# Optimization experiments

Measured on AMD Instinct MI355X. Metric: run time of the kernel, lower is better.

## Reference

```python
import jax, jax.numpy as jnp
import numpy as np

D_IN = 1024
D_OUT = 1024

def setup_inputs() -> dict:
    key = jax.random.key(0)
    ks = jax.random.split(key, 7)
    s = 1.0 / np.sqrt(D_IN)
    x = jax.random.normal(ks[0], (4, 2048, D_IN), dtype=jnp.float32)
    Wq = jax.random.uniform(ks[1], (D_IN, D_OUT), jnp.float32, -s, s)
    Wk = jax.random.uniform(ks[2], (D_IN, D_OUT), jnp.float32, -s, s)
    Wv = jax.random.uniform(ks[3], (D_IN, D_OUT), jnp.float32, -s, s)
    bq = jax.random.uniform(ks[4], (D_OUT,), jnp.float32, -s, s)
    bk = jax.random.uniform(ks[5], (D_OUT,), jnp.float32, -s, s)
    bv = jax.random.uniform(ks[6], (D_OUT,), jnp.float32, -s, s)
    return {"x": x, "Wq": Wq, "Wk": Wk, "Wv": Wv, "bq": bq, "bk": bk, "bv": bv}

def reference(x, Wq, Wk, Wv, bq, bk, bv):
    # x: [b, n, d_in]
    q = jnp.einsum('bnd,de->bne', x, Wq) + bq
    k = jnp.einsum('bnd,de->bne', x, Wk) + bk
    v = jnp.einsum('bnd,de->bne', x, Wv) + bv
    scale = 1.0 / jnp.sqrt(jnp.asarray(k.shape[-1], dtype=x.dtype))
    scores = jnp.einsum('bqe,bke->bqk', q, k) * scale  # [b, n, n]
    weights = jax.nn.softmax(scores, axis=-1)
    return jnp.einsum('bqk,bke->bqe', weights, v)
```

## Files before the change

kernel.cpp:

```cpp
#include <hip/hip_runtime.h>
#include <cstdint>

typedef __bf16 bf16x8 __attribute__((ext_vector_type(8)));
typedef float f32x16 __attribute__((ext_vector_type(16)));

__device__ __forceinline__ unsigned short f2b(float f) {
    union { float f; uint32_t u; } x; x.f = f;
    uint32_t r = (x.u + 0x7fffu + ((x.u >> 16) & 1u)) >> 16;
    return (unsigned short)r;
}
__device__ __forceinline__ float b2f(unsigned short h) {
    union { float f; uint32_t u; } x; x.u = ((uint32_t)h) << 16;
    return x.f;
}

__global__ __launch_bounds__(256) void prep_kernel(const float* __restrict__ x,
                                                   unsigned short* __restrict__ xb,
                                                   const float* __restrict__ Wq,
                                                   const float* __restrict__ Wk,
                                                   const float* __restrict__ Wv,
                                                   unsigned short* __restrict__ Wt) {
    const int bid = blockIdx.x;
    const int tid = threadIdx.x;
    if (bid < 8192) {
        int i = (bid * 256 + tid) * 4;
        float4 v = *(const float4*)(x + i);
        ushort4 o;
        o.x = f2b(v.x); o.y = f2b(v.y); o.z = f2b(v.z); o.w = f2b(v.w);
        *(ushort4*)(xb + i) = o;
    } else {
        __shared__ float tile[32][33];
        const int b = bid - 8192;
        const int z = b >> 10;
        const int rem = b & 1023;
        const int n0 = (rem & 31) * 32;
        const int k0 = (rem >> 5) * 32;
        const float* W = (z == 0) ? Wq : (z == 1) ? Wk : Wv;
        const int tx = tid & 31, ty4 = tid >> 5;
#pragma unroll
        for (int i = 0; i < 4; ++i)
            tile[ty4 * 4 + i][tx] = W[(k0 + ty4 * 4 + i) * 1024 + n0 + tx];
        __syncthreads();
#pragma unroll
        for (int i = 0; i < 4; ++i) {
            const int row = ty4 * 4 + i;
            Wt[((long)z * 1024 + n0 + row) * 1024 + k0 + tx] = f2b(tile[tx][row]);
        }
    }
}

template <int EPI>
__global__ __launch_bounds__(256) void gemm32(const unsigned short* __restrict__ A, int lda, long sA,
                                              const unsigned short* __restrict__ Bm, int ldb, long sB,
                                              void* __restrict__ Cv, long sC, int K,
                                              const float* __restrict__ bq, const float* __restrict__ bk,
                                              const float* __restrict__ bv,
                                              unsigned short* __restrict__ Qb,
                                              unsigned short* __restrict__ Kb,
                                              unsigned short* __restrict__ Vt) {
    __shared__ unsigned short As0[128 * 64];
    __shared__ unsigned short Bs0[128 * 64];
    __shared__ unsigned short As1[128 * 64];
    __shared__ unsigned short Bs1[128 * 64];

    const int tid = threadIdx.x;
    const int wave = tid >> 6, lane = tid & 63;
    const int h = lane >> 5;
    const int l31 = lane & 31;
    const int wm = wave >> 1, wn = wave & 1;
    const long bm = (long)blockIdx.y * 128;
    const long bn = (long)blockIdx.x * 128;

    const unsigned short* Ab = A + (long)blockIdx.z * sA;
    const unsigned short* Bb = Bm + (long)blockIdx.z * sB;

    f32x16 acc[2][2];
#pragma unroll
    for (int mi = 0; mi < 2; ++mi) {
#pragma unroll
        for (int ni = 0; ni < 2; ++ni) {
#pragma unroll
            for (int r = 0; r < 16; ++r) acc[mi][ni][r] = 0.0f;
        }
    }

    const int srow_in = lane >> 3;
    const int cswz = (lane & 7) ^ srow_in;
    const unsigned short* aptr[4];
    const unsigned short* bptr[4];
    int sloff[4];
#pragma unroll
    for (int j = 0; j < 4; ++j) {
        const int row = j * 32 + wave * 8 + srow_in;
        aptr[j] = Ab + (bm + row) * (long)lda + cswz * 8;
        bptr[j] = Bb + (bn + row) * (long)ldb + cswz * 8;
        sloff[j] = (j * 32 + wave * 8) * 64;
    }

    const int arow0 = (wm * 64 + l31) * 64;
    const int brow0 = (wn * 64 + l31) * 64;
    int sw[4];
#pragma unroll
    for (int kh = 0; kh < 4; ++kh)
        sw[kh] = (((2 * kh + h) ^ (lane & 7)) * 8);

#define STAGE(AsB, BsB, kofs)                                                                           \
    do {                                                                                                \
        _Pragma("unroll")                                                                               \
        for (int j = 0; j < 4; ++j) {                                                                   \
            __builtin_amdgcn_global_load_lds(                                                           \
                (const __attribute__((address_space(1))) void*)(aptr[j] + (kofs)),                      \
                (__attribute__((address_space(3))) void*)(&AsB[sloff[j]]), 16, 0, 0);                   \
            __builtin_amdgcn_global_load_lds(                                                           \
                (const __attribute__((address_space(1))) void*)(bptr[j] + (kofs)),                      \
                (__attribute__((address_space(3))) void*)(&BsB[sloff[j]]), 16, 0, 0);                   \
        }                                                                                               \
    } while (0)

#define COMPUTE_T(AsB, BsB)                                                                             \
    do {                                                                                                \
        _Pragma("unroll")                                                                               \
        for (int kp = 0; kp < 2; ++kp) {                                                                \
            bf16x8 af[2][2], bfr[2][2];                                                                 \
            _Pragma("unroll")                                                                           \
            for (int mi = 0; mi < 2; ++mi) {                                                            \
                _Pragma("unroll")                                                                       \
                for (int kk = 0; kk < 2; ++kk) {                                                        \
                    af[mi][kk] = *(const bf16x8*)&AsB[arow0 + mi * 32 * 64 + sw[kp * 2 + kk]];          \
                }                                                                                       \
            }                                                                                           \
            _Pragma("unroll")                                                                           \
            for (int ni = 0; ni < 2; ++ni) {                                                            \
                _Pragma("unroll")                                                                       \
                for (int kk = 0; kk < 2; ++kk) {                                                        \
                    bfr[ni][kk] = *(const bf16x8*)&BsB[brow0 + ni * 32 * 64 + sw[kp * 2 + kk]];         \
                }                                                                                       \
            }                                                                                           \
            _Pragma("unroll")                                                                           \
            for (int kk = 0; kk < 2; ++kk) {                                                            \
                _Pragma("unroll")                                                                       \
                for (int mi = 0; mi < 2; ++mi) {                                                        \
                    _Pragma("unroll")                                                                   \
                    for (int ni = 0; ni < 2; ++ni) {                                                    \
                        acc[mi][ni] = __builtin_amdgcn_mfma_f32_32x32x16_bf16(af[mi][kk], bfr[ni][kk],  \
                                                                              acc[mi][ni], 0, 0, 0);    \
                    }                                                                                   \
                }                                                                                       \
            }                                                                                           \
        }                                                                                               \
    } while (0)

    STAGE(As0, Bs0, 0);

    for (int k0 = 0; k0 < K; k0 += 128) {
        __syncthreads();
        STAGE(As1, Bs1, k0 + 64);
        COMPUTE_T(As0, Bs0);
        __syncthreads();
        if (k0 + 128 < K) STAGE(As0, Bs0, k0 + 128);
        COMPUTE_T(As1, Bs1);
    }

#undef STAGE
#undef COMPUTE_T

#pragma unroll
    for (int mi = 0; mi < 2; ++mi) {
#pragma unroll
        for (int ni = 0; ni < 2; ++ni) {
            const f32x16 a = acc[mi][ni];
            const long col = bn + wn * 64 + ni * 32 + l31;
            const long rowB = bm + wm * 64 + mi * 32 + h * 4;
            if constexpr (EPI == 0) {
                if (col < 1024) {
                    const float bias = bq[col];
#pragma unroll
                    for (int g = 0; g < 4; ++g) {
#pragma unroll
                        for (int r = 0; r < 4; ++r)
                            Qb[(rowB + g * 8 + r) * 1024 + col] = f2b((a[g * 4 + r] + bias) * 0.03125f);
                    }
                } else if (col < 2048) {
                    const float bias = bk[col - 1024];
#pragma unroll
                    for (int g = 0; g < 4; ++g) {
#pragma unroll
                        for (int r = 0; r < 4; ++r)
                            Kb[(rowB + g * 8 + r) * 1024 + (col - 1024)] = f2b(a[g * 4 + r] + bias);
                    }
                } else {
                    const float bias = bv[col - 2048];
#pragma unroll
                    for (int g = 0; g < 4; ++g) {
                        const long row0 = rowB + g * 8;
                        const long batch = row0 >> 11;
                        const int n = (int)(row0 & 2047);
                        ushort4 o;
                        o.x = f2b(a[g * 4 + 0] + bias);
                        o.y = f2b(a[g * 4 + 1] + bias);
                        o.z = f2b(a[g * 4 + 2] + bias);
                        o.w = f2b(a[g * 4 + 3] + bias);
                        *(ushort4*)&Vt[(batch * 1024 + (col - 2048)) * 2048 + n] = o;
                    }
                }
            } else if constexpr (EPI == 1) {
                unsigned short* S = (unsigned short*)Cv + (long)blockIdx.z * sC;
#pragma unroll
                for (int g = 0; g < 4; ++g) {
#pragma unroll
                    for (int r = 0; r < 4; ++r)
                        S[(rowB + g * 8 + r) * 2048 + col] = f2b(a[g * 4 + r]);
                }
            } else {
                float* O = (float*)Cv + (long)blockIdx.z * sC;
#pragma unroll
                for (int g = 0; g < 4; ++g) {
#pragma unroll
                    for (int r = 0; r < 4; ++r)
                        O[(rowB + g * 8 + r) * 1024 + col] = a[g * 4 + r];
                }
            }
        }
    }
}

__global__ __launch_bounds__(256) void softmax_kernel(unsigned short* __restrict__ S) {
    const long row = blockIdx.x;
    unsigned short* p = S + row * 2048;
    const int tid = threadIdx.x;
    const int wave = tid >> 6, lane = tid & 63;

    ushort4 u0 = *(const ushort4*)&p[tid * 8];
    ushort4 u1 = *(const ushort4*)&p[tid * 8 + 4];
    float v[8];
    v[0] = b2f(u0.x); v[1] = b2f(u0.y); v[2] = b2f(u0.z); v[3] = b2f(u0.w);
    v[4] = b2f(u1.x); v[5] = b2f(u1.y); v[6] = b2f(u1.z); v[7] = b2f(u1.w);

    float m = v[0];
#pragma unroll
    for (int j = 1; j < 8; ++j) m = fmaxf(m, v[j]);
#pragma unroll
    for (int off = 32; off; off >>= 1) m = fmaxf(m, __shfl_xor(m, off, 64));
    __shared__ float redm[4];
    __shared__ float reds[4];
    if (lane == 0) redm[wave] = m;
    __syncthreads();
    m = fmaxf(fmaxf(redm[0], redm[1]), fmaxf(redm[2], redm[3]));

    float s = 0.0f;
#pragma unroll
    for (int j = 0; j < 8; ++j) { v[j] = __expf(v[j] - m); s += v[j]; }
#pragma unroll
    for (int off = 32; off; off >>= 1) s += __shfl_xor(s, off, 64);
    if (lane == 0) reds[wave] = s;
    __syncthreads();
    s = reds[0] + reds[1] + reds[2] + reds[3];
    const float inv = 1.0f / s;

    u0.x = f2b(v[0] * inv); u0.y = f2b(v[1] * inv); u0.z = f2b(v[2] * inv); u0.w = f2b(v[3] * inv);
    u1.x = f2b(v[4] * inv); u1.y = f2b(v[5] * inv); u1.z = f2b(v[6] * inv); u1.w = f2b(v[7] * inv);
    *(ushort4*)&p[tid * 8] = u0;
    *(ushort4*)&p[tid * 8 + 4] = u1;
}

extern "C" void kernel_launch(void* const* d_in, const int* in_sizes, int n_in,
                              void* d_out, int out_size, void* d_ws, size_t ws_size,
                              hipStream_t stream) {
    const float* x  = (const float*)d_in[0];
    const float* Wq = (const float*)d_in[1];
    const float* Wk = (const float*)d_in[2];
    const float* Wv = (const float*)d_in[3];
    const float* bq = (const float*)d_in[4];
    const float* bk = (const float*)d_in[5];
    const float* bv = (const float*)d_in[6];
    float* out = (float*)d_out;

    char* ws = (char*)d_ws;
    unsigned short* xb = (unsigned short*)ws; ws += 8192L * 1024 * 2;
    unsigned short* Wt = (unsigned short*)ws; ws += 3072L * 1024 * 2;
    unsigned short* Qb = (unsigned short*)ws; ws += 8192L * 1024 * 2;
    unsigned short* Kb = (unsigned short*)ws; ws += 8192L * 1024 * 2;
    unsigned short* Vt = (unsigned short*)ws; ws += 4L * 1024 * 2048 * 2;
    unsigned short* S  = (unsigned short*)ws; ws += 4L * 2048 * 2048 * 2;

    prep_kernel<<<8192 + 3072, 256, 0, stream>>>(x, xb, Wq, Wk, Wv, Wt);
    gemm32<0><<<dim3(24, 64, 1), 256, 0, stream>>>(xb, 1024, 0, Wt, 1024, 0,
                                                   nullptr, 0, 1024, bq, bk, bv, Qb, Kb, Vt);
    gemm32<1><<<dim3(16, 16, 4), 256, 0, stream>>>(Qb, 1024, 2048L * 1024, Kb, 1024, 2048L * 1024,
                                                   S, 2048L * 2048, 1024,
                                                   nullptr, nullptr, nullptr, nullptr, nullptr, nullptr);
    softmax_kernel<<<8192, 256, 0, stream>>>(S);
    gemm32<2><<<dim3(8, 16, 4), 256, 0, stream>>>(S, 2048, 2048L * 2048, Vt, 2048, 2048L * 1024,
                                                  out, 2048L * 1024, 2048,
                                                  nullptr, nullptr, nullptr, nullptr, nullptr, nullptr);
}
```

Measured before the change: 259.1 us.

## Fuse softmax into QK and PV GEMM epilogues with deferred normalization

Removes the standalone softmax kernel. The QK^T epilogue now writes exp(scores) in bf16 and accumulates per-row sums with shuffles and atomicAdd into a zeroed buffer. The PV epilogue divides by the row sum. This saves a full read and write pass over the score matrix and one launch. In exchange it drops max subtraction, so it can overflow for large scores, and it adds atomic traffic.

```diff
diff --git a/kernel.cpp b/kernel.cpp
--- a/kernel.cpp
+++ b/kernel.cpp
@@ -19,7 +19,8 @@
                                                    const float* __restrict__ Wq,
                                                    const float* __restrict__ Wk,
                                                    const float* __restrict__ Wv,
-                                                   unsigned short* __restrict__ Wt) {
+                                                   unsigned short* __restrict__ Wt,
+                                                   float* __restrict__ rowsum) {
     const int bid = blockIdx.x;
     const int tid = threadIdx.x;
     if (bid < 8192) {
@@ -28,7 +29,7 @@
         ushort4 o;
         o.x = f2b(v.x); o.y = f2b(v.y); o.z = f2b(v.z); o.w = f2b(v.w);
         *(ushort4*)(xb + i) = o;
-    } else {
+    } else if (bid < 11264) {
         __shared__ float tile[32][33];
         const int b = bid - 8192;
         const int z = b >> 10;
@@ -46,6 +47,9 @@
             const int row = ty4 * 4 + i;
             Wt[((long)z * 1024 + n0 + row) * 1024 + k0 + tx] = f2b(tile[tx][row]);
         }
+    } else {
+#pragma unroll
+        for (int i = 0; i < 32; ++i) rowsum[i * 256 + tid] = 0.0f;
     }
 }
 
@@ -57,7 +61,8 @@
                                               const float* __restrict__ bv,
                                               unsigned short* __restrict__ Qb,
                                               unsigned short* __restrict__ Kb,
-                                              unsigned short* __restrict__ Vt) {
+                                              unsigned short* __restrict__ Vt,
+                                              float* __restrict__ rowsum) {
     __shared__ unsigned short As0[128 * 64];
     __shared__ unsigned short Bs0[128 * 64];
     __shared__ unsigned short As1[128 * 64];
@@ -164,14 +169,14 @@
 #undef STAGE
 #undef COMPUTE_T
 
-#pragma unroll
-    for (int mi = 0; mi < 2; ++mi) {
-#pragma unroll
-        for (int ni = 0; ni < 2; ++ni) {
-            const f32x16 a = acc[mi][ni];
-            const long col = bn + wn * 64 + ni * 32 + l31;
-            const long rowB = bm + wm * 64 + mi * 32 + h * 4;
-            if constexpr (EPI == 0) {
+    if constexpr (EPI == 0) {
+#pragma unroll
+        for (int mi = 0; mi < 2; ++mi) {
+#pragma unroll
+            for (int ni = 0; ni < 2; ++ni) {
+                const f32x16 a = acc[mi][ni];
+                const long col = bn + wn * 64 + ni * 32 + l31;
+                const long rowB = bm + wm * 64 + mi * 32 + h * 4;
                 if (col < 1024) {
                     const float bias = bq[col];
 #pragma unroll
@@ -203,64 +208,52 @@
                         *(ushort4*)&Vt[(batch * 1024 + (col - 2048)) * 2048 + n] = o;
                     }
                 }
-            } else if constexpr (EPI == 1) {
-                unsigned short* S = (unsigned short*)Cv + (long)blockIdx.z * sC;
-#pragma unroll
-                for (int g = 0; g < 4; ++g) {
-#pragma unroll
-                    for (int r = 0; r < 4; ++r)
-                        S[(rowB + g * 8 + r) * 2048 + col] = f2b(a[g * 4 + r]);
-                }
-            } else {
-                float* O = (float*)Cv + (long)blockIdx.z * sC;
-#pragma unroll
-                for (int g = 0; g < 4; ++g) {
-#pragma unroll
-                    for (int r = 0; r < 4; ++r)
-                        O[(rowB + g * 8 + r) * 1024 + col] = a[g * 4 + r];
+            }
+        }
+    } else if constexpr (EPI == 1) {
+        unsigned short* S = (unsigned short*)Cv + (long)blockIdx.z * sC;
+        float* rs = rowsum + (long)blockIdx.z * 2048;
+        const long c0 = bn + wn * 64 + l31;
+#pragma unroll
+        for (int mi = 0; mi < 2; ++mi) {
+            const long rB = bm + wm * 64 + mi * 32 + h * 4;
+#pragma unroll
+            for (int g = 0; g < 4; ++g) {
+#pragma unroll
+                for (int r = 0; r < 4; ++r) {
+                    const long row = rB + g * 8 + r;
+                    const float e0 = __expf(acc[mi][0][g * 4 + r]);
+                    const float e1 = __expf(acc[mi][1][g * 4 + r]);
+                    S[row * 2048 + c0] = f2b(e0);
+                    S[row * 2048 + c0 + 32] = f2b(e1);
+                    float es = e0 + e1;
+#pragma unroll
+                    for (int off = 16; off; off >>= 1) es += __shfl_xor(es, off, 64);
+                    if (l31 == 0) atomicAdd(&rs[row], es);
                 }
             }
         }
-    }
-}
-
-__global__ __launch_bounds__(256) void softmax_kernel(unsigned short* __restrict__ S) {
-    const long row = blockIdx.x;
-    unsigned short* p = S + row * 2048;
-    const int tid = threadIdx.x;
-    const int wave = tid >> 6, lane = tid & 63;
-
-    ushort4 u0 = *(const ushort4*)&p[tid * 8];
-    ushort4 u1 = *(const ushort4*)&p[tid * 8 + 4];
-    float v[8];
-    v[0] = b2f(u0.x); v[1] = b2f(u0.y); v[2] = b2f(u0.z); v[3] = b2f(u0.w);
-    v[4] = b2f(u1.x); v[5] = b2f(u1.y); v[6] = b2f(u1.z); v[7] = b2f(u1.w);
-
-    float m = v[0];
-#pragma unroll
-    for (int j = 1; j < 8; ++j) m = fmaxf(m, v[j]);
-#pragma unroll
-    for (int off = 32; off; off >>= 1) m = fmaxf(m, __shfl_xor(m, off, 64));
-    __shared__ float redm[4];
-    __shared__ float reds[4];
-    if (lane == 0) redm[wave] = m;
-    __syncthreads();
-    m = fmaxf(fmaxf(redm[0], redm[1]), fmaxf(redm[2], redm[3]));
-
-    float s = 0.0f;
-#pragma unroll
-    for (int j = 0; j < 8; ++j) { v[j] = __expf(v[j] - m); s += v[j]; }
-#pragma unroll
-    for (int off = 32; off; off >>= 1) s += __shfl_xor(s, off, 64);
-    if (lane == 0) reds[wave] = s;
-    __syncthreads();
-    s = reds[0] + reds[1] + reds[2] + reds[3];
-    const float inv = 1.0f / s;
-
-    u0.x = f2b(v[0] * inv); u0.y = f2b(v[1] * inv); u0.z = f2b(v[2] * inv); u0.w = f2b(v[3] * inv);
-    u1.x = f2b(v[4] * inv); u1.y = f2b(v[5] * inv); u1.z = f2b(v[6] * inv); u1.w = f2b(v[7] * inv);
-    *(ushort4*)&p[tid * 8] = u0;
-    *(ushort4*)&p[tid * 8 + 4] = u1;
+    } else {
+        float* O = (float*)Cv + (long)blockIdx.z * sC;
+        const float* rs = rowsum + (long)blockIdx.z * 2048;
+#pragma unroll
+        for (int mi = 0; mi < 2; ++mi) {
+            const long rB = bm + wm * 64 + mi * 32 + h * 4;
+#pragma unroll
+            for (int g = 0; g < 4; ++g) {
+#pragma unroll
+                for (int r = 0; r < 4; ++r) {
+                    const long row = rB + g * 8 + r;
+                    const float inv = 1.0f / rs[row];
+#pragma unroll
+                    for (int ni = 0; ni < 2; ++ni) {
+                        const long col = bn + wn * 64 + ni * 32 + l31;
+                        O[row * 1024 + col] = acc[mi][ni][g * 4 + r] * inv;
+                    }
+                }
+            }
+        }
+    }
 }
 
 extern "C" void kernel_launch(void* const* d_in, const int* in_sizes, int n_in,
@@ -282,15 +275,17 @@
     unsigned short* Kb = (unsigned short*)ws; ws += 8192L * 1024 * 2;
     unsigned short* Vt = (unsigned short*)ws; ws += 4L * 1024 * 2048 * 2;
     unsigned short* S  = (unsigned short*)ws; ws += 4L * 2048 * 2048 * 2;
-
-    prep_kernel<<<8192 + 3072, 256, 0, stream>>>(x, xb, Wq, Wk, Wv, Wt);
+    float* rowsum      = (float*)ws;          ws += 8192L * 4;
+
+    prep_kernel<<<8192 + 3072 + 1, 256, 0, stream>>>(x, xb, Wq, Wk, Wv, Wt, rowsum);
     gemm32<0><<<dim3(24, 64, 1), 256, 0, stream>>>(xb, 1024, 0, Wt, 1024, 0,
-                                                   nullptr, 0, 1024, bq, bk, bv, Qb, Kb, Vt);
+                                                   nullptr, 0, 1024, bq, bk, bv, Qb, Kb, Vt, nullptr);
     gemm32<1><<<dim3(16, 16, 4), 256, 0, stream>>>(Qb, 1024, 2048L * 1024, Kb, 1024, 2048L * 1024,
                                                    S, 2048L * 2048, 1024,
-                                                   nullptr, nullptr, nullptr, nullptr, nullptr, nullptr);
-    softmax_kernel<<<8192, 256, 0, stream>>>(S);
+                                                   nullptr, nullptr, nullptr, nullptr, nullptr, nullptr,
+                                                   rowsum);
     gemm32<2><<<dim3(8, 16, 4), 256, 0, stream>>>(S, 2048, 2048L * 2048, Vt, 2048, 2048L * 1024,
                                                   out, 2048L * 1024, 2048,
-                                                  nullptr, nullptr, nullptr, nullptr, nullptr, nullptr);
-}
+                                                  nullptr, nullptr, nullptr, nullptr, nullptr, nullptr,
+                                                  rowsum);
+}
```

After: 260.2 us. About the same (+0.4%).
